# Kernel tuning notes

Hardware: AMD Instinct MI355X
Metric: run time of the kernel (lower is better)

## Reference

```python
import jax, jax.numpy as jnp
import numpy as np
import math

B, N, DEG, D = 128, 512, 8, 128
E = B * N * DEG
K1 = math.ceil(0.8 * N)    # 410 nodes kept per graph after pool1
K2 = math.ceil(0.8 * K1)   # 328 nodes kept per graph after pool2


def setup_inputs() -> dict:
    key = jax.random.key(0)
    ks = jax.random.split(key, 24)
    x = jax.random.normal(ks[0], (B * N, D), jnp.float32)
    # random edges within each graph, then offset to global node ids
    src_l = jax.random.randint(ks[1], (B, N * DEG), 0, N)
    dst_l = jax.random.randint(ks[2], (B, N * DEG), 0, N)
    offs = (jnp.arange(B) * N)[:, None]
    edge_index = jnp.stack([(src_l + offs).reshape(-1), (dst_l + offs).reshape(-1)]).astype(jnp.int32)
    w = lambda k, s: (jax.random.normal(k, s, jnp.float32) * 0.05)
    return {
        "x": x, "edge_index": edge_index,
        "W1r": w(ks[3], (D, 128)), "W1n": w(ks[4], (D, 128)), "b1": jnp.zeros((128,), jnp.float32),
        "p1": w(ks[5], (128,)),
        "W2r": w(ks[6], (128, 128)), "W2n": w(ks[7], (128, 128)), "b2": jnp.zeros((128,), jnp.float32),
        "p2": w(ks[8], (128,)),
        "lw1": w(ks[9], (256, 128)), "lb1": jnp.zeros((128,), jnp.float32),
        "lw2": w(ks[10], (128, 64)), "lb2": jnp.zeros((64,), jnp.float32),
        "lw3": w(ks[11], (64, 1)), "lb3": jnp.zeros((1,), jnp.float32),
    }


def _conv(h, src, dst, Wr, Wn, b):
    # GraphConv-style spatio-temporal message passing, sum aggregation
    msg = h[src] @ Wn                                   # [E, 128]
    agg = jax.ops.segment_sum(msg, dst, num_segments=B * N)
    return h @ Wr + agg + b


def _topk_mask(score, k, prev_mask):
    # per-graph top-k node selection (TopKPooling); restrict to prev_mask
    s = jnp.where(prev_mask, score, -jnp.inf).reshape(B, N)
    idx = jax.lax.top_k(s, k)[1]                        # [B, k]
    m = jnp.zeros((B, N), bool).at[jnp.arange(B)[:, None], idx].set(True)
    return m.reshape(B * N)


def _readout(h, mask, k):
    # concat of global max pool and global mean pool over kept nodes
    hm = jnp.where(mask[:, None], h, -jnp.inf).reshape(B, N, -1)
    gmax = hm.max(axis=1)
    gmean = (h * mask[:, None].astype(h.dtype)).reshape(B, N, -1).sum(axis=1) / k
    return jnp.concatenate([gmax, gmean], axis=1)       # [B, 256]


def reference(x, edge_index, W1r, W1n, b1, p1, W2r, W2n, b2, p2, lw1, lb1, lw2, lb2, lw3, lb3):
    src, dst = edge_index[0], edge_index[1]
    # conv1 + relu
    h = jax.nn.relu(_conv(x, src, dst, W1r, W1n, b1))
    # pool1: score = h.p/||p||, keep top-K1, gate by tanh(score)
    s1 = h @ p1 / jnp.linalg.norm(p1)
    m1 = _topk_mask(s1, K1, jnp.ones(B * N, bool))
    h = h * (jnp.tanh(s1) * m1.astype(h.dtype))[:, None]
    x1 = _readout(h, m1, K1)
    # conv2 + relu (dropped nodes have zero features -> zero messages)
    h = jax.nn.relu(_conv(h, src, dst, W2r, W2n, b2))
    s2 = h @ p2 / jnp.linalg.norm(p2)
    m2 = _topk_mask(s2, K2, m1)
    h = h * (jnp.tanh(s2) * m2.astype(h.dtype))[:, None]
    x2 = _readout(h, m2, K2)
    # MLP head (bn1/bn2 are defined but unused in the original forward; dropout is eval-mode identity)
    z = x1 + x2
    z = jax.nn.relu(z @ lw1 + lb1)
    z = jax.nn.relu(z @ lw2 + lb2)
    return jax.nn.sigmoid(z @ lw3 + lb3).squeeze(-1)    # [B]
```

## Files before the change

### kernel.cpp

```cpp
#include <hip/hip_runtime.h>
#include <math.h>

constexpr int B = 128;
constexpr int N = 512;
constexpr int DEG = 8;
constexpr int D = 128;
constexpr int E = B * N * DEG;
constexpr int EPG = N * DEG;
constexpr int NN = B * N;
constexpr int K1 = 410;
constexpr int K2 = 328;
constexpr int PADDEG = 16;
constexpr int CAP = 32;

typedef __attribute__((ext_vector_type(8))) short short8;
typedef __attribute__((ext_vector_type(4))) float f32x4;

__device__ __forceinline__ unsigned short f2bf(float f) {
    unsigned int u = __float_as_uint(f);
    unsigned int r = (u + 0x7fffu + ((u >> 16) & 1u)) >> 16;
    return (unsigned short)r;
}
__device__ __forceinline__ float bf2f(unsigned short h) {
    return __uint_as_float(((unsigned int)h) << 16);
}

__global__ __launch_bounds__(256) void k_prepw(const float* __restrict__ W0,
                                               const float* __restrict__ W1,
                                               const float* __restrict__ W2,
                                               const float* __restrict__ W3,
                                               unsigned short* __restrict__ wt,
                                               int* __restrict__ ccnt) {
    const float* Ws[4] = {W0, W1, W2, W3};
    const int m = blockIdx.x >> 6;
    const int idx = (blockIdx.x & 63) * 256 + threadIdx.x;
    ccnt[blockIdx.x * 256 + threadIdx.x] = 0;
    const float* src = Ws[m];
    unsigned short* dH = wt + (size_t)m * 32768;
    unsigned short* dL = dH + 16384;
    int kk = idx >> 7, n = idx & 127;
    float v = src[idx];
    unsigned short h = f2bf(v);
    unsigned short l = f2bf(v - bf2f(h));
    dH[n * 128 + kk] = h;
    dL[n * 128 + kk] = l;
}

__global__ __launch_bounds__(256) void k_count(const int* __restrict__ ei,
                                               int* __restrict__ ccnt,
                                               int* __restrict__ csrcp) {
    const int e = blockIdx.x * 256 + threadIdx.x;
    const int s = ei[e];
    const int d = ei[E + e];
    const int pos = atomicAdd(&ccnt[d], 1);
    if (pos < CAP) csrcp[(size_t)d * CAP + pos] = s;
}

__global__ __launch_bounds__(256) void k_sortpad(int* __restrict__ ccnt,
                                                 int* __restrict__ csrcp) {
    const int n = blockIdx.x * 256 + threadIdx.x;
    const int deg = min(ccnt[n], CAP);
    int a[CAP];
    #pragma unroll
    for (int j = 0; j < CAP / 4; ++j)
        *(int4*)&a[4 * j] = *(const int4*)&csrcp[(size_t)n * CAP + 4 * j];
    #pragma unroll
    for (int k = 0; k < CAP; ++k)
        if (k >= deg) a[k] = 0x7fffffff;
    #pragma unroll
    for (int k = 2; k <= CAP; k <<= 1) {
        #pragma unroll
        for (int j = k >> 1; j > 0; j >>= 1) {
            #pragma unroll
            for (int i = 0; i < CAP; ++i) {
                const int l = i ^ j;
                if (l > i) {
                    const bool dir = ((i & k) == 0);
                    int x = a[i], y = a[l];
                    if ((x > y) == dir) { a[i] = y; a[l] = x; }
                }
            }
        }
    }
    #pragma unroll
    for (int j = 0; j < CAP / 4; ++j)
        *(int4*)&csrcp[(size_t)n * CAP + 4 * j] =
            make_int4(a[4 * j], a[4 * j + 1], a[4 * j + 2], a[4 * j + 3]);
}

__global__ __launch_bounds__(256, 2) void k_gather(const float* __restrict__ feat,
                                                   const float* __restrict__ gate,
                                                   const int* __restrict__ ccnt,
                                                   const int* __restrict__ csrcp,
                                                   float* __restrict__ aggout) {
    const int bid = blockIdx.x;
    const int xcd = bid & 7;
    const int j = bid >> 3;
    const int g = ((j & 15) << 3) | xcd;
    const int chunk = j >> 4;
    const int t = threadIdx.x;
    const int lane = t & 31, grp = t >> 5;
    const int fo = lane * 4;
    #pragma unroll
    for (int it = 0; it < 4; ++it) {
        const int n = g * N + chunk * 32 + it * 8 + grp;
        const int deg = min(ccnt[n], CAP);
        int idx[PADDEG];
        *(int4*)&idx[0]  = *(const int4*)&csrcp[(size_t)n * CAP + 0];
        *(int4*)&idx[4]  = *(const int4*)&csrcp[(size_t)n * CAP + 4];
        *(int4*)&idx[8]  = *(const int4*)&csrcp[(size_t)n * CAP + 8];
        *(int4*)&idx[12] = *(const int4*)&csrcp[(size_t)n * CAP + 12];
        float4 acc = make_float4(0.f, 0.f, 0.f, 0.f);
        #pragma unroll
        for (int k = 0; k < PADDEG; ++k) {
            if (k < deg) {
                float wk = gate ? gate[idx[k]] : 1.0f;
                float4 v = *(const float4*)&feat[(size_t)idx[k] * D + fo];
                acc.x = fmaf(v.x, wk, acc.x);
                acc.y = fmaf(v.y, wk, acc.y);
                acc.z = fmaf(v.z, wk, acc.z);
                acc.w = fmaf(v.w, wk, acc.w);
            }
        }
        if (deg > PADDEG) {
            for (int k = PADDEG; k < deg; ++k) {
                int ix = csrcp[(size_t)n * CAP + k];
                float gt = gate ? gate[ix] : 1.0f;
                float4 v = *(const float4*)&feat[(size_t)ix * D + fo];
                acc.x = fmaf(v.x, gt, acc.x);
                acc.y = fmaf(v.y, gt, acc.y);
                acc.z = fmaf(v.z, gt, acc.z);
                acc.w = fmaf(v.w, gt, acc.w);
            }
        }
        *(float4*)&aggout[(size_t)n * D + fo] = acc;
    }
}

__global__ __launch_bounds__(512, 2) void k_gemm(const float* __restrict__ A0,
                                                 const float* __restrict__ gateA,
                                                 const float* __restrict__ A1,
                                                 const unsigned short* __restrict__ W0t,
                                                 const unsigned short* __restrict__ W1t,
                                                 const float* __restrict__ bias,
                                                 const float* __restrict__ pvec,
                                                 float* __restrict__ out,
                                                 float* __restrict__ sun) {
    __shared__ unsigned short AsBuf[2 * 128 * 40];
    __shared__ unsigned short BsH[128 * 40], BsL[128 * 40];
    unsigned short* AsH = AsBuf;
    unsigned short* AsL = AsBuf + 128 * 40;
    float* red = (float*)AsBuf;
    const int t = threadIdx.x;
    const int r0 = blockIdx.x * 128;
    const int w = t >> 6, lane = t & 63;
    const int lr = lane & 15, kg = (lane >> 4) * 8;
    const int wm = (w >> 1) * 32, wn = (w & 1) * 64;
    const int arow = t >> 2, kpart = (t & 3) * 8;
    const float ga = gateA ? gateA[r0 + arow] : 1.0f;

    f32x4 acc[2][4];
    #pragma unroll
    for (int mt = 0; mt < 2; ++mt)
        #pragma unroll
        for (int nt = 0; nt < 4; ++nt)
            acc[mt][nt] = (f32x4)(0.f);

    for (int phase = 0; phase < 2; ++phase) {
        const float* Ap = phase ? A1 : A0;
        const unsigned short* WH = phase ? W1t : W0t;
        const unsigned short* WL = WH + 16384;
        const float gmul = phase ? 1.0f : ga;
        for (int c = 0; c < 4; ++c) {
            const int k0 = c * 32;
            __syncthreads();
            {
                float4 a0 = *(const float4*)&Ap[(size_t)(r0 + arow) * D + k0 + kpart];
                float4 a1 = *(const float4*)&Ap[(size_t)(r0 + arow) * D + k0 + kpart + 4];
                float vals[8] = {a0.x * gmul, a0.y * gmul, a0.z * gmul, a0.w * gmul,
                                 a1.x * gmul, a1.y * gmul, a1.z * gmul, a1.w * gmul};
                unsigned int ph[4], pl[4];
                #pragma unroll
                for (int jj = 0; jj < 4; ++jj) {
                    unsigned int h0 = f2bf(vals[2 * jj]), h1 = f2bf(vals[2 * jj + 1]);
                    ph[jj] = h0 | (h1 << 16);
                    unsigned int l0 = f2bf(vals[2 * jj] - bf2f((unsigned short)h0));
                    unsigned int l1 = f2bf(vals[2 * jj + 1] - bf2f((unsigned short)h1));
                    pl[jj] = l0 | (l1 << 16);
                }
                *(int4*)&AsH[arow * 40 + kpart] = make_int4(ph[0], ph[1], ph[2], ph[3]);
                *(int4*)&AsL[arow * 40 + kpart] = make_int4(pl[0], pl[1], pl[2], pl[3]);
            }
            *(int4*)&BsH[arow * 40 + kpart] = *(const int4*)&WH[arow * 128 + k0 + kpart];
            *(int4*)&BsL[arow * 40 + kpart] = *(const int4*)&WL[arow * 128 + k0 + kpart];
            __syncthreads();
            short8 aH[2], aL[2], bH[4], bL[4];
            #pragma unroll
            for (int mt = 0; mt < 2; ++mt) {
                aH[mt] = *(const short8*)&AsH[(wm + mt * 16 + lr) * 40 + kg];
                aL[mt] = *(const short8*)&AsL[(wm + mt * 16 + lr) * 40 + kg];
            }
            #pragma unroll
            for (int nt = 0; nt < 4; ++nt) {
                bH[nt] = *(const short8*)&BsH[(wn + nt * 16 + lr) * 40 + kg];
                bL[nt] = *(const short8*)&BsL[(wn + nt * 16 + lr) * 40 + kg];
            }
            #pragma unroll
            for (int mt = 0; mt < 2; ++mt)
                #pragma unroll
                for (int nt = 0; nt < 4; ++nt) {
                    acc[mt][nt] = __builtin_amdgcn_mfma_f32_16x16x32_bf16(aH[mt], bH[nt], acc[mt][nt], 0, 0, 0);
                    acc[mt][nt] = __builtin_amdgcn_mfma_f32_16x16x32_bf16(aH[mt], bL[nt], acc[mt][nt], 0, 0, 0);
                    acc[mt][nt] = __builtin_amdgcn_mfma_f32_16x16x32_bf16(aL[mt], bH[nt], acc[mt][nt], 0, 0, 0);
                }
        }
    }
    __syncthreads();
    float bb[4], pv[4];
    #pragma unroll
    for (int nt = 0; nt < 4; ++nt) {
        bb[nt] = bias[wn + nt * 16 + lr];
        pv[nt] = pvec[wn + nt * 16 + lr];
    }
    #pragma unroll
    for (int mt = 0; mt < 2; ++mt) {
        #pragma unroll
        for (int r = 0; r < 4; ++r) {
            const int rowl = wm + mt * 16 + (lane >> 4) * 4 + r;
            const int row = r0 + rowl;
            float part = 0.f;
            #pragma unroll
            for (int nt = 0; nt < 4; ++nt) {
                float v = acc[mt][nt][r] + bb[nt];
                v = fmaxf(v, 0.f);
                out[(size_t)row * D + wn + nt * 16 + lr] = v;
                part = fmaf(v, pv[nt], part);
            }
            red[rowl * 33 + (w & 1) * 16 + lr] = part;
        }
    }
    __syncthreads();
    if (t < 128) {
        float s = 0.f;
        #pragma unroll
        for (int j = 0; j < 32; ++j) s += red[t * 33 + j];
        sun[r0 + t] = s;
    }
}

__global__ __launch_bounds__(1024) void k_topk_readout(const float* __restrict__ sun,
                                                       const float* __restrict__ p,
                                                       const float* __restrict__ prevmask,
                                                       int K, float invK,
                                                       const float* __restrict__ h,
                                                       float* __restrict__ gate,
                                                       float* __restrict__ mask,
                                                       float* __restrict__ xout) {
    __shared__ float ls[512];
    __shared__ float lg[512];
    __shared__ float lm[512];
    __shared__ float red[128];
    __shared__ float smax[16][64];
    __shared__ float ssum[16][64];
    __shared__ float norm_s;
    const int bid = blockIdx.x;
    const int g = bid >> 1, half = bid & 1;
    const int t = threadIdx.x;
    if (t < 512) {
        const int n = g * N + t;
        float s = sun[n];
        if (prevmask && prevmask[n] == 0.0f) s = -INFINITY;
        ls[t] = s;
    }
    if (t < 128) { float pvv = p[t]; red[t] = pvv * pvv; }
    __syncthreads();
    if (t < 64) red[t] += red[t + 64];
    __syncthreads();
    if (t < 32) red[t] += red[t + 32];
    __syncthreads();
    if (t == 0) {
        float s = 0.f;
        #pragma unroll
        for (int i = 0; i < 32; ++i) s += red[i];
        norm_s = sqrtf(s);
    }
    __syncthreads();
    if (t < 512) {
        const float s = ls[t];
        int cnt = 0;
        for (int jj = 0; jj < 512; ++jj) {
            float sj = ls[jj];
            cnt += (sj > s || (sj == s && jj < t)) ? 1 : 0;
        }
        const bool keep = cnt < K;
        const float gv = keep ? tanhf(s / norm_s) : 0.0f;
        const float mv = keep ? 1.0f : 0.0f;
        lg[t] = gv; lm[t] = mv;
        gate[g * N + t] = gv; mask[g * N + t] = mv;
    }
    __syncthreads();
    const int f = half * 64 + (t & 63), sub = t >> 6;
    float vmax = -INFINITY, vsum = 0.f;
    for (int nl = sub; nl < N; nl += 16) {
        const float v = h[(size_t)(g * N + nl) * D + f] * lg[nl];
        vsum += v;
        if (lm[nl] != 0.f) vmax = fmaxf(vmax, v);
    }
    smax[sub][t & 63] = vmax;
    ssum[sub][t & 63] = vsum;
    __syncthreads();
    if (t < 64) {
        float m = smax[0][t], s = ssum[0][t];
        #pragma unroll
        for (int k = 1; k < 16; ++k) { m = fmaxf(m, smax[k][t]); s += ssum[k][t]; }
        xout[g * 256 + half * 64 + t] = m;
        xout[g * 256 + 128 + half * 64 + t] = s * invK;
    }
}

__global__ __launch_bounds__(128) void k_mlp(const float* __restrict__ X1,
                                             const float* __restrict__ X2,
                                             const float* __restrict__ lw1,
                                             const float* __restrict__ lb1,
                                             const float* __restrict__ lw2,
                                             const float* __restrict__ lb2,
                                             const float* __restrict__ lw3,
                                             const float* __restrict__ lb3,
                                             float* __restrict__ out) {
    __shared__ float z[256];
    __shared__ float o1[128];
    __shared__ float o2p[64];
    const int g = blockIdx.x, t = threadIdx.x;
    z[t] = X1[g * 256 + t] + X2[g * 256 + t];
    z[t + 128] = X1[g * 256 + 128 + t] + X2[g * 256 + 128 + t];
    __syncthreads();
    float a = lb1[t];
    for (int i = 0; i < 256; ++i) a = fmaf(z[i], lw1[i * 128 + t], a);
    o1[t] = fmaxf(a, 0.f);
    __syncthreads();
    if (t < 64) {
        float b = lb2[t];
        for (int i = 0; i < 128; ++i) b = fmaf(o1[i], lw2[i * 64 + t], b);
        o2p[t] = fmaxf(b, 0.f) * lw3[t];
    }
    __syncthreads();
    if (t == 0) {
        float sacc = lb3[0];
        for (int i = 0; i < 64; ++i) sacc += o2p[i];
        out[g] = 1.f / (1.f + expf(-sacc));
    }
}

extern "C" void kernel_launch(void* const* d_in, const int* in_sizes, int n_in,
                              void* d_out, int out_size, void* d_ws, size_t ws_size,
                              hipStream_t stream) {
    const float* x    = (const float*)d_in[0];
    const int*   ei   = (const int*)d_in[1];
    const float* W1r  = (const float*)d_in[2];
    const float* W1n  = (const float*)d_in[3];
    const float* b1   = (const float*)d_in[4];
    const float* p1   = (const float*)d_in[5];
    const float* W2r  = (const float*)d_in[6];
    const float* W2n  = (const float*)d_in[7];
    const float* b2   = (const float*)d_in[8];
    const float* p2   = (const float*)d_in[9];
    const float* lw1  = (const float*)d_in[10];
    const float* lb1  = (const float*)d_in[11];
    const float* lw2  = (const float*)d_in[12];
    const float* lb2  = (const float*)d_in[13];
    const float* lw3  = (const float*)d_in[14];
    const float* lb3  = (const float*)d_in[15];
    float* out = (float*)d_out;

    char* w = (char*)d_ws;
    float* h1  = (float*)w; w += (size_t)NN * D * 4;
    float* h2  = (float*)w; w += (size_t)NN * D * 4;
    float* agg = (float*)w; w += (size_t)NN * D * 4;
    int* ccnt  = (int*)w;   w += (size_t)NN * 4;
    int* csrcp = (int*)w;   w += (size_t)NN * CAP * 4;
    unsigned short* wt = (unsigned short*)w; w += (size_t)4 * 2 * 16384 * 2;
    float* sun = (float*)w; w += (size_t)NN * 4;
    float* g1  = (float*)w; w += (size_t)NN * 4;
    float* m1  = (float*)w; w += (size_t)NN * 4;
    float* g2  = (float*)w; w += (size_t)NN * 4;
    float* m2  = (float*)w; w += (size_t)NN * 4;
    float* X1  = (float*)w; w += (size_t)B * 256 * 4;
    float* X2  = (float*)w; w += (size_t)B * 256 * 4;

    const unsigned short* wt1r = wt;
    const unsigned short* wt1n = wt + 1 * 32768;
    const unsigned short* wt2r = wt + 2 * 32768;
    const unsigned short* wt2n = wt + 3 * 32768;

    k_prepw<<<256, 256, 0, stream>>>(W1r, W1n, W2r, W2n, wt, ccnt);
    k_count<<<E / 256, 256, 0, stream>>>(ei, ccnt, csrcp);
    k_sortpad<<<NN / 256, 256, 0, stream>>>(ccnt, csrcp);

    k_gather<<<2048, 256, 0, stream>>>(x, nullptr, ccnt, csrcp, agg);
    k_gemm<<<NN / 128, 512, 0, stream>>>(x, nullptr, agg, wt1r, wt1n, b1, p1, h1, sun);
    k_topk_readout<<<2 * B, 1024, 0, stream>>>(sun, p1, nullptr, K1, 1.0f / (float)K1, h1, g1, m1, X1);

    k_gather<<<2048, 256, 0, stream>>>(h1, g1, ccnt, csrcp, agg);
    k_gemm<<<NN / 128, 512, 0, stream>>>(h1, g1, agg, wt2r, wt2n, b2, p2, h2, sun);
    k_topk_readout<<<2 * B, 1024, 0, stream>>>(sun, p2, m1, K2, 1.0f / (float)K2, h2, g2, m2, X2);

    k_mlp<<<B, 128, 0, stream>>>(X1, X2, lw1, lb1, lw2, lb2, lw3, lb3, out);
}
```

Baseline: 284.1 us.

## Fuse neighbor gather into the GEMM A-tile load, dropping the agg buffer

Removes the separate gather kernel and the intermediate aggregation buffer. Each GEMM block now stages its rows' neighbor indices and gate weights in shared memory, then builds the phase-1 A tile by summing neighbor features on the fly. Blocks are remapped so one block covers 128 rows of a single graph, placed on an XCD-aware schedule. The LDS row stride changes from 40 to 36 with split int2 accesses, and the occupancy hint is raised. This avoids writing and re-reading a 32 MB aggregate, at the cost of per-neighbor latency-bound loads inside the GEMM loop and a variable-length, serialized loop that may stall the MFMA pipeline.

```diff
diff --git a/kernel.cpp b/kernel.cpp
--- a/kernel.cpp
+++ b/kernel.cpp
@@ -6,12 +6,12 @@
 constexpr int DEG = 8;
 constexpr int D = 128;
 constexpr int E = B * N * DEG;
-constexpr int EPG = N * DEG;
 constexpr int NN = B * N;
 constexpr int K1 = 410;
 constexpr int K2 = 328;
-constexpr int PADDEG = 16;
 constexpr int CAP = 32;
+constexpr int AST = 36;
+constexpr int LST = 33;
 
 typedef __attribute__((ext_vector_type(8))) short short8;
 typedef __attribute__((ext_vector_type(4))) float f32x4;
@@ -88,76 +88,54 @@
             make_int4(a[4 * j], a[4 * j + 1], a[4 * j + 2], a[4 * j + 3]);
 }
 
-__global__ __launch_bounds__(256, 2) void k_gather(const float* __restrict__ feat,
-                                                   const float* __restrict__ gate,
-                                                   const int* __restrict__ ccnt,
-                                                   const int* __restrict__ csrcp,
-                                                   float* __restrict__ aggout) {
+__global__ __launch_bounds__(512, 4) void k_fgemm(const float* __restrict__ feat,
+                                                  const float* __restrict__ gate,
+                                                  const int* __restrict__ ccnt,
+                                                  const int* __restrict__ csrcp,
+                                                  const unsigned short* __restrict__ W0t,
+                                                  const unsigned short* __restrict__ W1t,
+                                                  const float* __restrict__ bias,
+                                                  const float* __restrict__ pvec,
+                                                  float* __restrict__ out,
+                                                  float* __restrict__ sun) {
+    __shared__ unsigned short AsBuf[2 * 128 * AST];
+    __shared__ unsigned short BsH[128 * AST], BsL[128 * AST];
+    __shared__ unsigned short lidx[128 * LST];
+    __shared__ float lwk[128 * LST];
+    __shared__ int ldeg[128];
+    unsigned short* AsH = AsBuf;
+    unsigned short* AsL = AsBuf + 128 * AST;
+    float* red = (float*)AsBuf;
     const int bid = blockIdx.x;
-    const int xcd = bid & 7;
-    const int j = bid >> 3;
-    const int g = ((j & 15) << 3) | xcd;
-    const int chunk = j >> 4;
+    const int xcd = bid & 7, j = bid >> 3;
+    const int g = (j & 15) * 8 + xcd;
+    const int chunkRow = j >> 4;
+    const int r0 = g * N + chunkRow * 128;
     const int t = threadIdx.x;
-    const int lane = t & 31, grp = t >> 5;
-    const int fo = lane * 4;
-    #pragma unroll
-    for (int it = 0; it < 4; ++it) {
-        const int n = g * N + chunk * 32 + it * 8 + grp;
-        const int deg = min(ccnt[n], CAP);
-        int idx[PADDEG];
-        *(int4*)&idx[0]  = *(const int4*)&csrcp[(size_t)n * CAP + 0];
-        *(int4*)&idx[4]  = *(const int4*)&csrcp[(size_t)n * CAP + 4];
-        *(int4*)&idx[8]  = *(const int4*)&csrcp[(size_t)n * CAP + 8];
-        *(int4*)&idx[12] = *(const int4*)&csrcp[(size_t)n * CAP + 12];
-        float4 acc = make_float4(0.f, 0.f, 0.f, 0.f);
-        #pragma unroll
-        for (int k = 0; k < PADDEG; ++k) {
-            if (k < deg) {
-                float wk = gate ? gate[idx[k]] : 1.0f;
-                float4 v = *(const float4*)&feat[(size_t)idx[k] * D + fo];
-                acc.x = fmaf(v.x, wk, acc.x);
-                acc.y = fmaf(v.y, wk, acc.y);
-                acc.z = fmaf(v.z, wk, acc.z);
-                acc.w = fmaf(v.w, wk, acc.w);
-            }
-        }
-        if (deg > PADDEG) {
-            for (int k = PADDEG; k < deg; ++k) {
-                int ix = csrcp[(size_t)n * CAP + k];
-                float gt = gate ? gate[ix] : 1.0f;
-                float4 v = *(const float4*)&feat[(size_t)ix * D + fo];
-                acc.x = fmaf(v.x, gt, acc.x);
-                acc.y = fmaf(v.y, gt, acc.y);
-                acc.z = fmaf(v.z, gt, acc.z);
-                acc.w = fmaf(v.w, gt, acc.w);
-            }
-        }
-        *(float4*)&aggout[(size_t)n * D + fo] = acc;
-    }
-}
-
-__global__ __launch_bounds__(512, 2) void k_gemm(const float* __restrict__ A0,
-                                                 const float* __restrict__ gateA,
-                                                 const float* __restrict__ A1,
-                                                 const unsigned short* __restrict__ W0t,
-                                                 const unsigned short* __restrict__ W1t,
-                                                 const float* __restrict__ bias,
-                                                 const float* __restrict__ pvec,
-                                                 float* __restrict__ out,
-                                                 float* __restrict__ sun) {
-    __shared__ unsigned short AsBuf[2 * 128 * 40];
-    __shared__ unsigned short BsH[128 * 40], BsL[128 * 40];
-    unsigned short* AsH = AsBuf;
-    unsigned short* AsL = AsBuf + 128 * 40;
-    float* red = (float*)AsBuf;
-    const int t = threadIdx.x;
-    const int r0 = blockIdx.x * 128;
     const int w = t >> 6, lane = t & 63;
     const int lr = lane & 15, kg = (lane >> 4) * 8;
     const int wm = (w >> 1) * 32, wn = (w & 1) * 64;
     const int arow = t >> 2, kpart = (t & 3) * 8;
-    const float ga = gateA ? gateA[r0 + arow] : 1.0f;
+    const int node = r0 + arow;
+    const float ga = gate ? gate[node] : 1.0f;
+
+    {
+        const int q = t & 3;
+        const int deg = min(ccnt[node], CAP);
+        if (q == 0) ldeg[arow] = deg;
+        int4 i0 = *(const int4*)&csrcp[(size_t)node * CAP + q * 8];
+        int4 i1 = *(const int4*)&csrcp[(size_t)node * CAP + q * 8 + 4];
+        int ids[8] = {i0.x, i0.y, i0.z, i0.w, i1.x, i1.y, i1.z, i1.w};
+        #pragma unroll
+        for (int u = 0; u < 8; ++u) {
+            const int slot = q * 8 + u;
+            lidx[arow * LST + slot] = (unsigned short)ids[u];
+            float wv = 0.f;
+            if (slot < deg) wv = gate ? gate[ids[u]] : 1.0f;
+            lwk[arow * LST + slot] = wv;
+        }
+    }
+    __syncthreads();
 
     f32x4 acc[2][4];
     #pragma unroll
@@ -167,18 +145,33 @@
             acc[mt][nt] = (f32x4)(0.f);
 
     for (int phase = 0; phase < 2; ++phase) {
-        const float* Ap = phase ? A1 : A0;
         const unsigned short* WH = phase ? W1t : W0t;
         const unsigned short* WL = WH + 16384;
-        const float gmul = phase ? 1.0f : ga;
         for (int c = 0; c < 4; ++c) {
             const int k0 = c * 32;
             __syncthreads();
+            float vals[8];
+            if (phase == 0) {
+                float4 a0 = *(const float4*)&feat[(size_t)node * D + k0 + kpart];
+                float4 a1 = *(const float4*)&feat[(size_t)node * D + k0 + kpart + 4];
+                vals[0] = a0.x * ga; vals[1] = a0.y * ga; vals[2] = a0.z * ga; vals[3] = a0.w * ga;
+                vals[4] = a1.x * ga; vals[5] = a1.y * ga; vals[6] = a1.z * ga; vals[7] = a1.w * ga;
+            } else {
+                #pragma unroll
+                for (int u = 0; u < 8; ++u) vals[u] = 0.f;
+                const int deg = ldeg[arow];
+                for (int k = 0; k < deg; ++k) {
+                    const int ix = lidx[arow * LST + k];
+                    const float wv = lwk[arow * LST + k];
+                    float4 v0 = *(const float4*)&feat[(size_t)ix * D + k0 + kpart];
+                    float4 v1 = *(const float4*)&feat[(size_t)ix * D + k0 + kpart + 4];
+                    vals[0] = fmaf(v0.x, wv, vals[0]); vals[1] = fmaf(v0.y, wv, vals[1]);
+                    vals[2] = fmaf(v0.z, wv, vals[2]); vals[3] = fmaf(v0.w, wv, vals[3]);
+                    vals[4] = fmaf(v1.x, wv, vals[4]); vals[5] = fmaf(v1.y, wv, vals[5]);
+                    vals[6] = fmaf(v1.z, wv, vals[6]); vals[7] = fmaf(v1.w, wv, vals[7]);
+                }
+            }
             {
-                float4 a0 = *(const float4*)&Ap[(size_t)(r0 + arow) * D + k0 + kpart];
-                float4 a1 = *(const float4*)&Ap[(size_t)(r0 + arow) * D + k0 + kpart + 4];
-                float vals[8] = {a0.x * gmul, a0.y * gmul, a0.z * gmul, a0.w * gmul,
-                                 a1.x * gmul, a1.y * gmul, a1.z * gmul, a1.w * gmul};
                 unsigned int ph[4], pl[4];
                 #pragma unroll
                 for (int jj = 0; jj < 4; ++jj) {
@@ -188,22 +181,36 @@
                     unsigned int l1 = f2bf(vals[2 * jj + 1] - bf2f((unsigned short)h1));
                     pl[jj] = l0 | (l1 << 16);
                 }
-                *(int4*)&AsH[arow * 40 + kpart] = make_int4(ph[0], ph[1], ph[2], ph[3]);
-                *(int4*)&AsL[arow * 40 + kpart] = make_int4(pl[0], pl[1], pl[2], pl[3]);
-            }
-            *(int4*)&BsH[arow * 40 + kpart] = *(const int4*)&WH[arow * 128 + k0 + kpart];
-            *(int4*)&BsL[arow * 40 + kpart] = *(const int4*)&WL[arow * 128 + k0 + kpart];
+                *(int2*)&AsH[arow * AST + kpart]     = make_int2(ph[0], ph[1]);
+                *(int2*)&AsH[arow * AST + kpart + 4] = make_int2(ph[2], ph[3]);
+                *(int2*)&AsL[arow * AST + kpart]     = make_int2(pl[0], pl[1]);
+                *(int2*)&AsL[arow * AST + kpart + 4] = make_int2(pl[2], pl[3]);
+            }
+            {
+                int4 bh = *(const int4*)&WH[arow * 128 + k0 + kpart];
+                int4 bl = *(const int4*)&WL[arow * 128 + k0 + kpart];
+                *(int2*)&BsH[arow * AST + kpart]     = make_int2(bh.x, bh.y);
+                *(int2*)&BsH[arow * AST + kpart + 4] = make_int2(bh.z, bh.w);
+                *(int2*)&BsL[arow * AST + kpart]     = make_int2(bl.x, bl.y);
+                *(int2*)&BsL[arow * AST + kpart + 4] = make_int2(bl.z, bl.w);
+            }
             __syncthreads();
             short8 aH[2], aL[2], bH[4], bL[4];
             #pragma unroll
             for (int mt = 0; mt < 2; ++mt) {
-                aH[mt] = *(const short8*)&AsH[(wm + mt * 16 + lr) * 40 + kg];
-                aL[mt] = *(const short8*)&AsL[(wm + mt * 16 + lr) * 40 + kg];
+                const int ra = (wm + mt * 16 + lr) * AST + kg;
+                ((int2*)&aH[mt])[0] = *(const int2*)&AsH[ra];
+                ((int2*)&aH[mt])[1] = *(const int2*)&AsH[ra + 4];
+                ((int2*)&aL[mt])[0] = *(const int2*)&AsL[ra];
+                ((int2*)&aL[mt])[1] = *(const int2*)&AsL[ra + 4];
             }
             #pragma unroll
             for (int nt = 0; nt < 4; ++nt) {
-                bH[nt] = *(const short8*)&BsH[(wn + nt * 16 + lr) * 40 + kg];
-                bL[nt] = *(const short8*)&BsL[(wn + nt * 16 + lr) * 40 + kg];
+                const int rb = (wn + nt * 16 + lr) * AST + kg;
+                ((int2*)&bH[nt])[0] = *(const int2*)&BsH[rb];
+                ((int2*)&bH[nt])[1] = *(const int2*)&BsH[rb + 4];
+                ((int2*)&bL[nt])[0] = *(const int2*)&BsL[rb];
+                ((int2*)&bL[nt])[1] = *(const int2*)&BsL[rb + 4];
             }
             #pragma unroll
             for (int mt = 0; mt < 2; ++mt)
@@ -243,7 +250,7 @@
     if (t < 128) {
         float s = 0.f;
         #pragma unroll
-        for (int j = 0; j < 32; ++j) s += red[t * 33 + j];
+        for (int jj = 0; jj < 32; ++jj) s += red[t * 33 + jj];
         sun[r0 + t] = s;
     }
 }
@@ -375,7 +382,6 @@
     char* w = (char*)d_ws;
     float* h1  = (float*)w; w += (size_t)NN * D * 4;
     float* h2  = (float*)w; w += (size_t)NN * D * 4;
-    float* agg = (float*)w; w += (size_t)NN * D * 4;
     int* ccnt  = (int*)w;   w += (size_t)NN * 4;
     int* csrcp = (int*)w;   w += (size_t)NN * CAP * 4;
     unsigned short* wt = (unsigned short*)w; w += (size_t)4 * 2 * 16384 * 2;
@@ -396,12 +402,10 @@
     k_count<<<E / 256, 256, 0, stream>>>(ei, ccnt, csrcp);
     k_sortpad<<<NN / 256, 256, 0, stream>>>(ccnt, csrcp);
 
-    k_gather<<<2048, 256, 0, stream>>>(x, nullptr, ccnt, csrcp, agg);
-    k_gemm<<<NN / 128, 512, 0, stream>>>(x, nullptr, agg, wt1r, wt1n, b1, p1, h1, sun);
+    k_fgemm<<<512, 512, 0, stream>>>(x, nullptr, ccnt, csrcp, wt1r, wt1n, b1, p1, h1, sun);
     k_topk_readout<<<2 * B, 1024, 0, stream>>>(sun, p1, nullptr, K1, 1.0f / (float)K1, h1, g1, m1, X1);
 
-    k_gather<<<2048, 256, 0, stream>>>(h1, g1, ccnt, csrcp, agg);
-    k_gemm<<<NN / 128, 512, 0, stream>>>(h1, g1, agg, wt2r, wt2n, b2, p2, h2, sun);
+    k_fgemm<<<512, 512, 0, stream>>>(h1, g1, ccnt, csrcp, wt2r, wt2n, b2, p2, h2, sun);
     k_topk_readout<<<2 * B, 1024, 0, stream>>>(sun, p2, m1, K2, 1.0f / (float)K2, h2, g2, m2, X2);
 
     k_mlp<<<B, 128, 0, stream>>>(X1, X2, lw1, lb1, lw2, lb2, lw3, lb3, out);
```

Result: faster. 265.1 us (median of 2 runs) (-6.7%).
